# Performance work log

Measured on AMD Instinct MI355X. Metric: run time of the kernel, lower is better.

Reference implementation:

```python
import jax, jax.numpy as jnp
import numpy as np

E, B, C_IN, H, W = 4, 32, 64, 64, 64
C_OUT, KH, KW = 128, 3, 3


def setup_inputs() -> dict:
    key = jax.random.key(0)
    k1, k2 = jax.random.split(key)
    features = jax.random.normal(k1, (E, B, C_IN, H, W), dtype=jnp.float32)
    # weight: ensemble + (in, out) + kernel, Glorot-style std = out_channels**-0.5
    weight = jax.random.normal(k2, (E, C_IN, C_OUT, KH, KW), dtype=jnp.float32) * (C_OUT ** -0.5)
    bias = jnp.zeros((E, C_OUT), dtype=jnp.float32)
    return {"features": features, "weight": weight, "bias": bias}


def reference(features, weight, bias):
    # features: (E, B, C_in, H, W); weight: (E, C_in, C_out, KH, KW); bias: (E, C_out)
    # The torch module's unfold+einsum equals a VALID cross-correlation per ensemble member:
    # out[e,b,j,y,x] = sum_{i,A,B} features[e,b,i,y+A,x+B] * weight[e,i,j,A,B]
    def conv_one(x, w):
        k = jnp.transpose(w, (1, 0, 2, 3))  # (C_out, C_in, KH, KW) = OIHW
        return jax.lax.conv_general_dilated(
            x, k, window_strides=(1, 1), padding="VALID",
            dimension_numbers=("NCHW", "OIHW", "NCHW"))

    out = jax.vmap(conv_one)(features, weight)  # (E, B, C_out, H', W')
    out = out + bias[:, None, :, None, None]
    return out
```

## Files before the change

kernel.cpp:

```cpp
#include <hip/hip_runtime.h>

typedef __bf16 bf16x8 __attribute__((ext_vector_type(8)));
typedef __bf16 bf16x2 __attribute__((ext_vector_type(2)));
typedef float  f32x4  __attribute__((ext_vector_type(4)));

#define FT_BYTES 67108864ull

__device__ __forceinline__ void gl2lds16(const void* g, void* l) {
    __builtin_amdgcn_global_load_lds(
        (const __attribute__((address_space(1))) void*)g,
        (__attribute__((address_space(3))) void*)l, 16, 0, 0);
}

__global__ void wt_prep(const float* __restrict__ w, __bf16* __restrict__ wt) {
    int o = blockIdx.x * 256 + threadIdx.x;
    int i = o & 63, j = (o >> 6) & 127, et = o >> 13;
    int tap = et % 9, e = et / 9;
    wt[o] = (__bf16)w[((e * 64 + i) * 128 + j) * 9 + tap];
}

__global__ void ft_prep(const float* __restrict__ f, __bf16* __restrict__ ft) {
    __shared__ float s[64 * 65];
    int eb = blockIdx.z * 32 + blockIdx.y, y = blockIdx.x;
    const float* src = f + (size_t)eb * 262144 + y * 64;
    int t = threadIdx.x;
    for (int r = 0; r < 4; ++r) {
        int f4 = r * 256 + t;
        int i = f4 >> 4, x4 = (f4 & 15) * 4;
        float4 v = *(const float4*)(src + i * 4096 + x4);
        s[i * 65 + x4 + 0] = v.x; s[i * 65 + x4 + 1] = v.y;
        s[i * 65 + x4 + 2] = v.z; s[i * 65 + x4 + 3] = v.w;
    }
    __syncthreads();
    bf16x2* dst = (bf16x2*)(ft + (size_t)(eb * 64 + y) * 4096);
    for (int r = 0; r < 8; ++r) {
        int q = r * 256 + t;
        int x = q >> 5, ih = q & 31;
        bf16x2 pv;
        pv.x = (__bf16)s[(2 * ih + 0) * 65 + x];
        pv.y = (__bf16)s[(2 * ih + 1) * 65 + x];
        dst[q] = pv;
    }
}

__global__ __launch_bounds__(256, 2)
void conv_main(const __bf16* __restrict__ ft, const __bf16* __restrict__ wt,
               const float* __restrict__ bias, float* __restrict__ out) {
    __shared__ __align__(16) __bf16 sA[128 * 64];
    __shared__ __align__(16) __bf16 sB[128 * 64];
    const int e = blockIdx.z, b = blockIdx.y, y0 = blockIdx.x * 2;
    const int eb = e * 32 + b;
    const int t = threadIdx.x, lane = t & 63, w = t >> 6;
    const int wm = w >> 1, wn = w & 1;
    const int q = lane >> 4, rm = lane & 15;

    f32x4 acc[4][4] = {};
    const __bf16* ftb = ft + (size_t)eb * 262144;

    for (int tap = 0; tap < 9; ++tap) {
        const int A = tap / 3, Bt = tap - A * 3;
        __syncthreads();
        const __bf16* wtap = wt + ((size_t)(e * 9 + tap) << 13);
        for (int cc = 0; cc < 4; ++cc) {
            int c = w * 4 + cc;
            int r = c * 8 + (lane >> 3);
            int g = (lane & 7) ^ (r & 7);
            gl2lds16(wtap + r * 64 + g * 8, sA + c * 512);
        }
        const int yA = y0 + A;
        for (int cc = 0; cc < 4; ++cc) {
            int c = w * 4 + cc;
            int p = c * 8 + (lane >> 3);
            int py = p >> 6, px = p & 63;
            int xx = px + Bt; if (xx > 63) xx = 63;
            int g = (lane & 7) ^ (p & 7);
            gl2lds16(ftb + (((yA + py) * 64 + xx) << 6) + g * 8, sB + c * 512);
        }
        __syncthreads();
        for (int kk = 0; kk < 64; kk += 32) {
            const int kg = kk >> 3;
            bf16x8 af[4], bq[4];
            for (int mi = 0; mi < 4; ++mi) {
                int r = wm * 64 + mi * 16 + rm;
                int ch = (kg + q) ^ (r & 7);
                af[mi] = *(const bf16x8*)(sA + r * 64 + ch * 8);
            }
            for (int ni = 0; ni < 4; ++ni) {
                int r = wn * 64 + ni * 16 + rm;
                int ch = (kg + q) ^ (r & 7);
                bq[ni] = *(const bf16x8*)(sB + r * 64 + ch * 8);
            }
            for (int mi = 0; mi < 4; ++mi)
                for (int ni = 0; ni < 4; ++ni)
                    acc[mi][ni] = __builtin_amdgcn_mfma_f32_16x16x32_bf16(
                        af[mi], bq[ni], acc[mi][ni], 0, 0, 0);
        }
    }

    for (int mi = 0; mi < 4; ++mi) {
        for (int ni = 0; ni < 4; ++ni) {
            int p = wn * 64 + ni * 16 + rm;
            int py = p >> 6, px = p & 63;
            if (px >= 62) continue;
            for (int vv = 0; vv < 4; ++vv) {
                int j = wm * 64 + mi * 16 + q * 4 + vv;
                float v = acc[mi][ni][vv] + bias[e * 128 + j];
                out[(((size_t)eb * 128 + j) * 62 + (y0 + py)) * 62 + px] = v;
            }
        }
    }
}

extern "C" void kernel_launch(void* const* d_in, const int* in_sizes, int n_in,
                              void* d_out, int out_size, void* d_ws, size_t ws_size,
                              hipStream_t stream) {
    const float* f    = (const float*)d_in[0];
    const float* wgt  = (const float*)d_in[1];
    const float* bias = (const float*)d_in[2];
    float* out = (float*)d_out;
    __bf16* ftw = (__bf16*)d_ws;
    __bf16* wtw = (__bf16*)((char*)d_ws + FT_BYTES);

    ft_prep<<<dim3(64, 32, 4), 256, 0, stream>>>(f, ftw);
    wt_prep<<<dim3(1152), 256, 0, stream>>>(wgt, wtw);
    conv_main<<<dim3(31, 32, 4), 256, 0, stream>>>(ftw, wtw, bias, out);
}
```

Before: 426.8 us.

## Reuse one feature tile across three horizontal taps and double-buffer loads

Each kernel row A now loads the feature tile once instead of three times. The x-shifted taps are served by offsetting the pixel row index inside LDS, since pixels are laid out as LDS rows. The feature tile is double-buffered so the next row's load overlaps the current MFMA work, and the three weight taps of a row are staged together. This cuts global-to-LDS traffic and the number of barriers. In exchange LDS use per block rises to about 80 KB, which may limit occupancy to the two blocks per CU the launch bounds request.

```diff
diff --git a/kernel.cpp b/kernel.cpp
--- a/kernel.cpp
+++ b/kernel.cpp
@@ -46,8 +46,8 @@
 __global__ __launch_bounds__(256, 2)
 void conv_main(const __bf16* __restrict__ ft, const __bf16* __restrict__ wt,
                const float* __restrict__ bias, float* __restrict__ out) {
-    __shared__ __align__(16) __bf16 sA[128 * 64];
-    __shared__ __align__(16) __bf16 sB[128 * 64];
+    __shared__ __align__(16) __bf16 sA[3 * 8192];
+    __shared__ __align__(16) __bf16 sB[2][8192];
     const int e = blockIdx.z, b = blockIdx.y, y0 = blockIdx.x * 2;
     const int eb = e * 32 + b;
     const int t = threadIdx.x, lane = t & 63, w = t >> 6;
@@ -56,44 +56,63 @@
 
     f32x4 acc[4][4] = {};
     const __bf16* ftb = ft + (size_t)eb * 262144;
+    const __bf16* wte = wt + ((size_t)(e * 9) << 13);
 
-    for (int tap = 0; tap < 9; ++tap) {
-        const int A = tap / 3, Bt = tap - A * 3;
-        __syncthreads();
-        const __bf16* wtap = wt + ((size_t)(e * 9 + tap) << 13);
-        for (int cc = 0; cc < 4; ++cc) {
-            int c = w * 4 + cc;
-            int r = c * 8 + (lane >> 3);
-            int g = (lane & 7) ^ (r & 7);
-            gl2lds16(wtap + r * 64 + g * 8, sA + c * 512);
+    auto stageA = [&](int A) {
+        for (int tp = 0; tp < 3; ++tp) {
+            const __bf16* wtap = wte + ((size_t)(A * 3 + tp) << 13);
+            for (int cc = 0; cc < 4; ++cc) {
+                int c = w * 4 + cc;
+                int r = c * 8 + (lane >> 3);
+                int g = (lane & 7) ^ (r & 7);
+                gl2lds16(wtap + r * 64 + g * 8, sA + tp * 8192 + c * 512);
+            }
         }
+    };
+    auto stageB = [&](int A, int buf) {
         const int yA = y0 + A;
         for (int cc = 0; cc < 4; ++cc) {
             int c = w * 4 + cc;
             int p = c * 8 + (lane >> 3);
             int py = p >> 6, px = p & 63;
-            int xx = px + Bt; if (xx > 63) xx = 63;
             int g = (lane & 7) ^ (p & 7);
-            gl2lds16(ftb + (((yA + py) * 64 + xx) << 6) + g * 8, sB + c * 512);
+            gl2lds16(ftb + (((yA + py) * 64 + px) << 6) + g * 8, sB[buf] + c * 512);
         }
+    };
+
+    stageA(0);
+    stageB(0, 0);
+
+    for (int A = 0; A < 3; ++A) {
+        const int buf = A & 1;
         __syncthreads();
-        for (int kk = 0; kk < 64; kk += 32) {
-            const int kg = kk >> 3;
-            bf16x8 af[4], bq[4];
-            for (int mi = 0; mi < 4; ++mi) {
-                int r = wm * 64 + mi * 16 + rm;
-                int ch = (kg + q) ^ (r & 7);
-                af[mi] = *(const bf16x8*)(sA + r * 64 + ch * 8);
+        if (A < 2) stageB(A + 1, buf ^ 1);
+        #pragma unroll 1
+        for (int tp = 0; tp < 3; ++tp) {
+            const __bf16* sAt = sA + tp * 8192;
+            for (int kk = 0; kk < 64; kk += 32) {
+                const int kg = kk >> 3;
+                bf16x8 af[4], bq[4];
+                for (int mi = 0; mi < 4; ++mi) {
+                    int r = wm * 64 + mi * 16 + rm;
+                    int ch = (kg + q) ^ (r & 7);
+                    af[mi] = *(const bf16x8*)(sAt + r * 64 + ch * 8);
+                }
+                for (int ni = 0; ni < 4; ++ni) {
+                    int r2 = wn * 64 + ni * 16 + rm + tp;
+                    if (r2 > 127) r2 = 127;
+                    int ch = (kg + q) ^ (r2 & 7);
+                    bq[ni] = *(const bf16x8*)(sB[buf] + r2 * 64 + ch * 8);
+                }
+                for (int mi = 0; mi < 4; ++mi)
+                    for (int ni = 0; ni < 4; ++ni)
+                        acc[mi][ni] = __builtin_amdgcn_mfma_f32_16x16x32_bf16(
+                            af[mi], bq[ni], acc[mi][ni], 0, 0, 0);
             }
-            for (int ni = 0; ni < 4; ++ni) {
-                int r = wn * 64 + ni * 16 + rm;
-                int ch = (kg + q) ^ (r & 7);
-                bq[ni] = *(const bf16x8*)(sB + r * 64 + ch * 8);
-            }
-            for (int mi = 0; mi < 4; ++mi)
-                for (int ni = 0; ni < 4; ++ni)
-                    acc[mi][ni] = __builtin_amdgcn_mfma_f32_16x16x32_bf16(
-                        af[mi], bq[ni], acc[mi][ni], 0, 0, 0);
+        }
+        if (A < 2) {
+            __syncthreads();
+            stageA(A + 1);
         }
     }
 
```

New measurement: 422.2 us. About the same (-1.1%).

## Load input rows into LDS once and stream weights through registers

Applied to the files above, without the earlier changes.

The conv kernel now loads the four input rows a block needs into a single shared buffer once, instead of re-gathering a shifted feature tile for each of the nine taps. Weight fragments are read straight from global memory into registers and double-buffered, prefetching the next tap's weights while the current tap's MFMAs run. This removes the per-tap barriers and the LDS staging of weights. In exchange it raises register pressure with the extra fragment buffers, and the weight loads from global or L2 are less coalesced.

```diff
diff --git a/kernel.cpp b/kernel.cpp
--- a/kernel.cpp
+++ b/kernel.cpp
@@ -46,8 +46,7 @@
 __global__ __launch_bounds__(256, 2)
 void conv_main(const __bf16* __restrict__ ft, const __bf16* __restrict__ wt,
                const float* __restrict__ bias, float* __restrict__ out) {
-    __shared__ __align__(16) __bf16 sA[128 * 64];
-    __shared__ __align__(16) __bf16 sB[128 * 64];
+    __shared__ __align__(16) __bf16 sF[256 * 64];
     const int e = blockIdx.z, b = blockIdx.y, y0 = blockIdx.x * 2;
     const int eb = e * 32 + b;
     const int t = threadIdx.x, lane = t & 63, w = t >> 6;
@@ -55,47 +54,64 @@
     const int q = lane >> 4, rm = lane & 15;
 
     f32x4 acc[4][4] = {};
-    const __bf16* ftb = ft + (size_t)eb * 262144;
+    const __bf16* ftb = ft + (size_t)eb * 262144 + ((size_t)y0 << 12);
+    const __bf16* wbase = wt + ((size_t)(e * 9) << 13)
+                        + (wm * 64 + rm) * 64 + q * 8;
 
-    for (int tap = 0; tap < 9; ++tap) {
+    for (int cc = 0; cc < 8; ++cc) {
+        int c = w * 8 + cc;
+        int r = c * 8 + (lane >> 3);
+        int g = (lane & 7) ^ (r & 7);
+        gl2lds16(ftb + (r << 6) + g * 8, sF + c * 512);
+    }
+
+    bf16x8 afA[8], afB[8];
+    #pragma unroll
+    for (int mi = 0; mi < 4; ++mi)
+        #pragma unroll
+        for (int kh = 0; kh < 2; ++kh)
+            afA[mi * 2 + kh] = *(const bf16x8*)(wbase + mi * 1024 + kh * 32);
+
+    __syncthreads();
+
+    auto body = [&](int tap, bf16x8* cur, bf16x8* nxt) {
+        if (tap < 8) {
+            const __bf16* wp = wbase + ((size_t)(tap + 1) << 13);
+            #pragma unroll
+            for (int mi = 0; mi < 4; ++mi)
+                #pragma unroll
+                for (int kh = 0; kh < 2; ++kh)
+                    nxt[mi * 2 + kh] = *(const bf16x8*)(wp + mi * 1024 + kh * 32);
+        }
         const int A = tap / 3, Bt = tap - A * 3;
-        __syncthreads();
-        const __bf16* wtap = wt + ((size_t)(e * 9 + tap) << 13);
-        for (int cc = 0; cc < 4; ++cc) {
-            int c = w * 4 + cc;
-            int r = c * 8 + (lane >> 3);
-            int g = (lane & 7) ^ (r & 7);
-            gl2lds16(wtap + r * 64 + g * 8, sA + c * 512);
-        }
-        const int yA = y0 + A;
-        for (int cc = 0; cc < 4; ++cc) {
-            int c = w * 4 + cc;
-            int p = c * 8 + (lane >> 3);
-            int py = p >> 6, px = p & 63;
-            int xx = px + Bt; if (xx > 63) xx = 63;
-            int g = (lane & 7) ^ (p & 7);
-            gl2lds16(ftb + (((yA + py) * 64 + xx) << 6) + g * 8, sB + c * 512);
-        }
-        __syncthreads();
-        for (int kk = 0; kk < 64; kk += 32) {
-            const int kg = kk >> 3;
-            bf16x8 af[4], bq[4];
-            for (int mi = 0; mi < 4; ++mi) {
-                int r = wm * 64 + mi * 16 + rm;
-                int ch = (kg + q) ^ (r & 7);
-                af[mi] = *(const bf16x8*)(sA + r * 64 + ch * 8);
+        #pragma unroll
+        for (int kh = 0; kh < 2; ++kh) {
+            const int kg = kh * 4;
+            bf16x8 bq[4];
+            #pragma unroll
+            for (int ni = 0; ni < 4; ++ni) {
+                int p = wn * 64 + ni * 16 + rm;
+                int py = p >> 6, px = p & 63;
+                int xx = px + Bt; if (xx > 63) xx = 63;
+                int r2 = (A + py) * 64 + xx;
+                int ch = (kg + q) ^ (r2 & 7);
+                bq[ni] = *(const bf16x8*)(sF + r2 * 64 + ch * 8);
             }
-            for (int ni = 0; ni < 4; ++ni) {
-                int r = wn * 64 + ni * 16 + rm;
-                int ch = (kg + q) ^ (r & 7);
-                bq[ni] = *(const bf16x8*)(sB + r * 64 + ch * 8);
-            }
+            #pragma unroll
             for (int mi = 0; mi < 4; ++mi)
+                #pragma unroll
                 for (int ni = 0; ni < 4; ++ni)
                     acc[mi][ni] = __builtin_amdgcn_mfma_f32_16x16x32_bf16(
-                        af[mi], bq[ni], acc[mi][ni], 0, 0, 0);
+                        cur[mi * 2 + kh], bq[ni], acc[mi][ni], 0, 0, 0);
         }
+    };
+
+    #pragma unroll 1
+    for (int tt = 0; tt < 4; ++tt) {
+        body(2 * tt,     afA, afB);
+        body(2 * tt + 1, afB, afA);
     }
+    body(8, afA, afB);
 
     for (int mi = 0; mi < 4; ++mi) {
         for (int ni = 0; ni < 4; ++ni) {
```

Measured after the change: 498.8 us. 1.17x slower.

## Keep per-member weights resident in LDS and double-buffer batch feature tiles

Applied to the files above, without the earlier changes.

Each 512-thread block loads all 9 taps for half of the output channels into LDS once. It then loops over 16 batch images, double-buffering a 4-row feature tile per image with async global-to-LDS loads. The 9 taps are applied through shifted LDS indexing, so weights and features are no longer reloaded from global memory once per tap. In exchange, LDS use per block grows to about 136KB, which limits residency to one block per CU. The grid shrinks to 496 blocks, and each wave holds a small 2x2 MFMA tile, which lowers the ratio of MFMA work to LDS reads.

```diff
diff --git a/kernel.cpp b/kernel.cpp
--- a/kernel.cpp
+++ b/kernel.cpp
@@ -43,71 +43,101 @@
     }
 }
 
-__global__ __launch_bounds__(256, 2)
+__global__ __launch_bounds__(512, 2)
 void conv_main(const __bf16* __restrict__ ft, const __bf16* __restrict__ wt,
                const float* __restrict__ bias, float* __restrict__ out) {
-    __shared__ __align__(16) __bf16 sA[128 * 64];
-    __shared__ __align__(16) __bf16 sB[128 * 64];
-    const int e = blockIdx.z, b = blockIdx.y, y0 = blockIdx.x * 2;
-    const int eb = e * 32 + b;
+    __shared__ __align__(16) __bf16 sW[9 * 4096];
+    __shared__ __align__(16) __bf16 sF[2][16384];
+    const int y0 = blockIdx.x * 2, jh = blockIdx.y;
+    const int e = blockIdx.z >> 1, bg = blockIdx.z & 1;
     const int t = threadIdx.x, lane = t & 63, w = t >> 6;
-    const int wm = w >> 1, wn = w & 1;
+    const int wm = w >> 2, wn = w & 3;
     const int q = lane >> 4, rm = lane & 15;
 
-    f32x4 acc[4][4] = {};
-    const __bf16* ftb = ft + (size_t)eb * 262144;
-
-    for (int tap = 0; tap < 9; ++tap) {
-        const int A = tap / 3, Bt = tap - A * 3;
-        __syncthreads();
-        const __bf16* wtap = wt + ((size_t)(e * 9 + tap) << 13);
-        for (int cc = 0; cc < 4; ++cc) {
-            int c = w * 4 + cc;
-            int r = c * 8 + (lane >> 3);
-            int g = (lane & 7) ^ (r & 7);
-            gl2lds16(wtap + r * 64 + g * 8, sA + c * 512);
-        }
-        const int yA = y0 + A;
-        for (int cc = 0; cc < 4; ++cc) {
-            int c = w * 4 + cc;
-            int p = c * 8 + (lane >> 3);
-            int py = p >> 6, px = p & 63;
-            int xx = px + Bt; if (xx > 63) xx = 63;
-            int g = (lane & 7) ^ (p & 7);
-            gl2lds16(ftb + (((yA + py) * 64 + xx) << 6) + g * 8, sB + c * 512);
-        }
-        __syncthreads();
-        for (int kk = 0; kk < 64; kk += 32) {
-            const int kg = kk >> 3;
-            bf16x8 af[4], bq[4];
-            for (int mi = 0; mi < 4; ++mi) {
-                int r = wm * 64 + mi * 16 + rm;
-                int ch = (kg + q) ^ (r & 7);
-                af[mi] = *(const bf16x8*)(sA + r * 64 + ch * 8);
-            }
-            for (int ni = 0; ni < 4; ++ni) {
-                int r = wn * 64 + ni * 16 + rm;
-                int ch = (kg + q) ^ (r & 7);
-                bq[ni] = *(const bf16x8*)(sB + r * 64 + ch * 8);
-            }
-            for (int mi = 0; mi < 4; ++mi)
-                for (int ni = 0; ni < 4; ++ni)
-                    acc[mi][ni] = __builtin_amdgcn_mfma_f32_16x16x32_bf16(
-                        af[mi], bq[ni], acc[mi][ni], 0, 0, 0);
-        }
+    const __bf16* wte = wt + ((size_t)(e * 9) << 13) + (jh << 12);
+    for (int k = 0; k < 9; ++k) {
+        int s = w * 9 + k;
+        int tap = s >> 3;
+        int r = (s & 7) * 8 + (lane >> 3);
+        int g = (lane & 7) ^ (r & 7);
+        gl2lds16(wte + (tap << 13) + r * 64 + g * 8, sW + s * 512);
+    }
+    const __bf16* fte = ft + ((size_t)(e * 32 + bg * 16) << 18) + ((size_t)y0 << 12);
+    for (int cc = 0; cc < 4; ++cc) {
+        int c = w * 4 + cc;
+        int r = c * 8 + (lane >> 3);
+        int g = (lane & 7) ^ (r & 7);
+        gl2lds16(fte + (r << 6) + g * 8, sF[0] + c * 512);
     }
 
-    for (int mi = 0; mi < 4; ++mi) {
-        for (int ni = 0; ni < 4; ++ni) {
-            int p = wn * 64 + ni * 16 + rm;
-            int py = p >> 6, px = p & 63;
-            if (px >= 62) continue;
-            for (int vv = 0; vv < 4; ++vv) {
-                int j = wm * 64 + mi * 16 + q * 4 + vv;
-                float v = acc[mi][ni][vv] + bias[e * 128 + j];
-                out[(((size_t)eb * 128 + j) * 62 + (y0 + py)) * 62 + px] = v;
+    float bias_r[2][4];
+    for (int mi = 0; mi < 2; ++mi)
+        for (int vv = 0; vv < 4; ++vv)
+            bias_r[mi][vv] = bias[e * 128 + jh * 64 + wm * 32 + mi * 16 + q * 4 + vv];
+
+    __syncthreads();
+
+    #pragma unroll 1
+    for (int it = 0; it < 16; ++it) {
+        const int buf = it & 1;
+        const __bf16* sFb = sF[buf];
+        if (it < 15) {
+            const __bf16* fn = fte + (((size_t)(it + 1)) << 18);
+            for (int cc = 0; cc < 4; ++cc) {
+                int c = w * 4 + cc;
+                int r = c * 8 + (lane >> 3);
+                int g = (lane & 7) ^ (r & 7);
+                gl2lds16(fn + (r << 6) + g * 8, sF[buf ^ 1] + c * 512);
             }
         }
+
+        f32x4 acc[2][2] = {};
+        #pragma unroll
+        for (int tap = 0; tap < 9; ++tap) {
+            const int A = tap / 3, Bt = tap - A * 3;
+            const __bf16* sWt = sW + tap * 4096;
+            #pragma unroll
+            for (int kh = 0; kh < 2; ++kh) {
+                const int kg = kh * 4;
+                bf16x8 af[2], bq[2];
+                #pragma unroll
+                for (int mi = 0; mi < 2; ++mi) {
+                    int r = wm * 32 + mi * 16 + rm;
+                    int ch = (kg + q) ^ (r & 7);
+                    af[mi] = *(const bf16x8*)(sWt + r * 64 + ch * 8);
+                }
+                #pragma unroll
+                for (int ni = 0; ni < 2; ++ni) {
+                    int p = wn * 32 + ni * 16 + rm;
+                    int py = p >> 6, px = p & 63;
+                    int xx = px + Bt; if (xx > 63) xx = 63;
+                    int r2 = (A + py) * 64 + xx;
+                    int ch = (kg + q) ^ (r2 & 7);
+                    bq[ni] = *(const bf16x8*)(sFb + r2 * 64 + ch * 8);
+                }
+                #pragma unroll
+                for (int mi = 0; mi < 2; ++mi)
+                    #pragma unroll
+                    for (int ni = 0; ni < 2; ++ni)
+                        acc[mi][ni] = __builtin_amdgcn_mfma_f32_16x16x32_bf16(
+                            af[mi], bq[ni], acc[mi][ni], 0, 0, 0);
+            }
+        }
+
+        const size_t eb = (size_t)(e * 32 + bg * 16 + it);
+        for (int mi = 0; mi < 2; ++mi) {
+            for (int ni = 0; ni < 2; ++ni) {
+                int p = wn * 32 + ni * 16 + rm;
+                int py = p >> 6, px = p & 63;
+                if (px >= 62) continue;
+                for (int vv = 0; vv < 4; ++vv) {
+                    int j = jh * 64 + wm * 32 + mi * 16 + q * 4 + vv;
+                    float v = acc[mi][ni][vv] + bias_r[mi][vv];
+                    out[((eb * 128 + j) * 62 + (y0 + py)) * 62 + px] = v;
+                }
+            }
+        }
+        if (it < 15) __syncthreads();
     }
 }
 
@@ -123,5 +153,5 @@
 
     ft_prep<<<dim3(64, 32, 4), 256, 0, stream>>>(f, ftw);
     wt_prep<<<dim3(1152), 256, 0, stream>>>(wgt, wtw);
-    conv_main<<<dim3(31, 32, 4), 256, 0, stream>>>(ftw, wtw, bias, out);
+    conv_main<<<dim3(31, 2, 8), 512, 0, stream>>>(ftw, wtw, bias, out);
 }
```

Result: no change. 424.1 us (-0.6%).
